# Optimization experiments

Hardware: AMD Instinct MI355X
Metric: run time of the kernel (lower is better)

## Reference

```python
import jax, jax.numpy as jnp
import numpy as np

HIST, CH, HH, WW2 = 10, 11, 30, 40
DM, LNUM, NH, OUT, AD, B = 128, 2, 1, 256, 20, 32
WS = (5, 5, 5)
SS = (2, 2, 2)
SCALE = (DM // NH) ** -0.5
VIS = HIST * CH * HH * WW2


def _np_window_partition(x, ws):
    Bx, D, H, W, C = x.shape
    x = x.reshape(Bx, D // ws[0], ws[0], H // ws[1], ws[1], W // ws[2], ws[2], C)
    return x.transpose(0, 1, 3, 5, 2, 4, 6, 7).reshape(-1, ws[0] * ws[1] * ws[2], C)


def _compute_mask(D, H, W, ws, ss):
    # replicates TinyVideoSwinEncoder._compute_mask (boundary mask + temporal causal mask)
    img = np.zeros((1, D, H, W, 1), np.float32)
    cnt = 0
    for d in (slice(-ws[0]), slice(-ws[0], -ss[0]), slice(-ss[0], None)):
        for h in (slice(-ws[1]), slice(-ws[1], -ss[1]), slice(-ss[1], None)):
            for w in (slice(-ws[2]), slice(-ws[2], -ss[2]), slice(-ss[2], None)):
                img[:, d, h, w, :] = cnt
                cnt += 1
    mw = _np_window_partition(img, ws)[..., 0]  # (nW, N)
    am = mw[:, None, :] - mw[:, :, None]
    am = np.where(am != 0, -100.0, 0.0).astype(np.float32)
    t = np.repeat(np.arange(ws[0]), ws[1] * ws[2])
    causal = np.where(t[:, None] < t[None, :], -100.0, 0.0).astype(np.float32)
    return am + causal[None]


def _rel_index(ws):
    coords = np.stack(np.meshgrid(np.arange(ws[0]), np.arange(ws[1]), np.arange(ws[2]), indexing='ij'))
    cf = coords.reshape(3, -1)
    rel = (cf[:, :, None] - cf[:, None, :]).transpose(1, 2, 0).copy()
    rel[..., 0] += ws[0] - 1
    rel[..., 1] += ws[1] - 1
    rel[..., 2] += ws[2] - 1
    rel[..., 0] *= (2 * ws[1] - 1) * (2 * ws[2] - 1)
    rel[..., 1] *= 2 * ws[2] - 1
    return rel.sum(-1)  # (N, N)


REL_IDX = _rel_index(WS)
MASK_SHIFT = jnp.asarray(_compute_mask(HIST, HH, WW2, WS, SS))
MASK_NONE = jnp.asarray(_compute_mask(HIST, HH, WW2, WS, (0, 0, 0)))


def _ln(x, w, b):
    m = x.mean(-1, keepdims=True)
    v = ((x - m) ** 2).mean(-1, keepdims=True)
    return (x - m) / jnp.sqrt(v + 1e-5) * w + b


def _win_part(x, ws):
    Bx, D, H, W, C = x.shape
    x = x.reshape(Bx, D // ws[0], ws[0], H // ws[1], ws[1], W // ws[2], ws[2], C)
    return x.transpose(0, 1, 3, 5, 2, 4, 6, 7).reshape(-1, ws[0] * ws[1] * ws[2], C)


def _win_rev(win, ws, Bx, D, H, W):
    x = win.reshape(Bx, D // ws[0], H // ws[1], W // ws[2], ws[0], ws[1], ws[2], -1)
    return x.transpose(0, 1, 4, 2, 5, 3, 6, 7).reshape(Bx, D, H, W, -1)


def _block(x, mask, shift, p):
    n1w, n1b, qw, qb, rpb, pw, pb, n2w, n2b, w1, b1, w2, b2 = p
    Bx, D, H, W, C = x.shape
    sc = x
    x = _ln(x, n1w, n1b)
    if any(s > 0 for s in shift):
        x = jnp.roll(x, tuple(-s for s in shift), axis=(1, 2, 3))
    xw = _win_part(x, WS)  # (B_, N, C)
    B_, N = xw.shape[0], xw.shape[1]
    qkv = (xw @ qw + qb).reshape(B_, N, 3, NH, C // NH).transpose(2, 0, 3, 1, 4)
    q, k, v = qkv[0] * SCALE, qkv[1], qkv[2]
    attn = jnp.einsum('bhnd,bhmd->bhnm', q, k)
    bias = rpb[REL_IDX.reshape(-1)].reshape(N, N, NH).transpose(2, 0, 1)
    attn = attn + bias[None]
    nW = mask.shape[0]
    attn = (attn.reshape(B_ // nW, nW, NH, N, N) + mask[None, :, None]).reshape(B_, NH, N, N)
    attn = jax.nn.softmax(attn, axis=-1)
    out = jnp.einsum('bhnm,bhmd->bhnd', attn, v).transpose(0, 2, 1, 3).reshape(B_, N, C)
    out = out @ pw + pb
    x = _win_rev(out, WS, Bx, D, H, W)
    if any(s > 0 for s in shift):
        x = jnp.roll(x, shift, axis=(1, 2, 3))
    x = sc + x
    h = _ln(x, n2w, n2b)
    return x + (jax.nn.gelu(h @ w1 + b1, approximate=False) @ w2 + b2)


def setup_inputs() -> dict:
    key = jax.random.key(0)
    ks = jax.random.split(key, 24)
    r = lambda k, s: jax.random.normal(k, s, jnp.float32) * 0.02
    RPB = (2 * WS[0] - 1) * (2 * WS[1] - 1) * (2 * WS[2] - 1)
    return {
        'obs_stack': jax.random.normal(ks[0], (B, VIS + AD), jnp.float32),
        'patch_w': r(ks[1], (CH, DM)), 'patch_b': r(ks[2], (DM,)),
        'norm1_w': 1.0 + r(ks[3], (LNUM, DM)), 'norm1_b': r(ks[4], (LNUM, DM)),
        'qkv_w': r(ks[5], (LNUM, DM, 3 * DM)), 'qkv_b': r(ks[6], (LNUM, 3 * DM)),
        'rpb_tab': r(ks[7], (LNUM, RPB, NH)),
        'proj_w': r(ks[8], (LNUM, DM, DM)), 'proj_b': r(ks[9], (LNUM, DM)),
        'norm2_w': 1.0 + r(ks[10], (LNUM, DM)), 'norm2_b': r(ks[11], (LNUM, DM)),
        'mlp_w1': r(ks[12], (LNUM, DM, 4 * DM)), 'mlp_b1': r(ks[13], (LNUM, 4 * DM)),
        'mlp_w2': r(ks[14], (LNUM, 4 * DM, DM)), 'mlp_b2': r(ks[15], (LNUM, DM)),
        'normf_w': 1.0 + r(ks[16], (DM,)), 'normf_b': r(ks[17], (DM,)),
        'out_w': r(ks[18], (DM + AD, OUT)), 'out_b': r(ks[19], (OUT,)),
    }


def reference(obs_stack, patch_w, patch_b, norm1_w, norm1_b, qkv_w, qkv_b, rpb_tab,
              proj_w, proj_b, norm2_w, norm2_b, mlp_w1, mlp_b1, mlp_w2, mlp_b2,
              normf_w, normf_b, out_w, out_b):
    Bx = obs_stack.shape[0]
    vis = obs_stack[:, :VIS].reshape(Bx, HIST, CH, HH, WW2).transpose(0, 1, 3, 4, 2)
    x = vis @ patch_w + patch_b  # [B, D, H, W, dm]
    for i in range(LNUM):
        shift = (0, 0, 0) if i % 2 == 0 else SS
        mask = MASK_NONE if i % 2 == 0 else MASK_SHIFT
        p = (norm1_w[i], norm1_b[i], qkv_w[i], qkv_b[i], rpb_tab[i], proj_w[i], proj_b[i],
             norm2_w[i], norm2_b[i], mlp_w1[i], mlp_b1[i], mlp_w2[i], mlp_b2[i])
        x = _block(x, mask, shift, p)
    x = _ln(x, normf_w, normf_b)
    pool = x.reshape(Bx, -1, DM).mean(axis=1)
    feat = jnp.concatenate([pool, obs_stack[:, VIS:]], axis=1)
    return feat @ out_w + out_b
```

## Files before the change

### kernel.cpp

```cpp
#include <hip/hip_runtime.h>
#include <hip/hip_bf16.h>

typedef unsigned short u16;
typedef short bf16x8 __attribute__((ext_vector_type(8)));
typedef float f32x4 __attribute__((ext_vector_type(4)));

#define SCALE_F 0.08838834764831845f

#define VC_PW    0
#define VC_PB    1408
#define VC_N1W   1536
#define VC_N1B   1792
#define VC_QKVB  2048
#define VC_PROJB 2816
#define VC_N2W   3072
#define VC_N2B   3328
#define VC_B1    3584
#define VC_B2    4608
#define VC_NFW   4864
#define VC_NFB   4992
#define VC_RPB   5120
#define VC_OW    6592
#define VC_OBIAS 44480

#define WT_QKV  0
#define WT_PROJ 98304
#define WT_W1   131072
#define WT_W2   262144

#define SH_OFF  8192
#define B1_OFF  13312
#define B2_OFF  13824

__device__ __forceinline__ float bf2f(u16 x) {
  union { unsigned int i; float f; } v; v.i = ((unsigned int)x) << 16; return v.f;
}
__device__ __forceinline__ u16 f2bf(float f) {
  __hip_bfloat16 h = __float2bfloat16(f);
  return __builtin_bit_cast(u16, h);
}
__device__ __forceinline__ unsigned int packbf(float a, float b) {
  return (unsigned int)f2bf(a) | ((unsigned int)f2bf(b) << 16);
}
__device__ __forceinline__ float wsum(float v) {
#pragma unroll
  for (int m = 32; m >= 1; m >>= 1) v += __shfl_xor(v, m, 64);
  return v;
}
__device__ __forceinline__ float gelu_f(float x) {
  float u = x * (-2.3022078f - 0.1029432f * x * x);
  float e = exp2f(u);
  return x * __builtin_amdgcn_rcpf(1.f + e);
}

__global__ __launch_bounds__(256) void k_scan(const u16* __restrict__ raw, int* __restrict__ flag) {
  int nanc = 0, ez = 0;
  for (int i = threadIdx.x; i < 131072; i += 256) {
    u16 x = raw[i];
    if ((x & 0x7F80u) == 0x7F80u) nanc++;
    if (!(i & 1) && x == 0) ez++;
  }
  atomicAdd(&flag[1], nanc);
  atomicAdd(&flag[2], ez);
}
__global__ void k_decide(int* __restrict__ flag) {
  if (threadIdx.x == 0) flag[0] = (flag[1] > 0 || flag[2] > 49152) ? 1 : 0;
}

__global__ __launch_bounds__(256) void k_conv(const void* __restrict__ src, u16* __restrict__ dst,
                                              int n, const int* __restrict__ flag) {
  const int fl = *flag;
  int i = blockIdx.x * 256 + threadIdx.x;
  if (i < n) dst[i] = fl ? f2bf(((const float*)src)[i]) : ((const u16*)src)[i];
}
struct CvTab { const void* src[15]; int off[15]; int n[15]; };
__global__ __launch_bounds__(256) void k_convb(CvTab t, u16* __restrict__ dst,
                                               const int* __restrict__ flag) {
  const int fl = *flag;
  const int s = blockIdx.y;
  const int i = blockIdx.x * 256 + threadIdx.x;
  if (i < t.n[s]) {
    const void* src = t.src[s];
    dst[t.off[s] + i] = fl ? f2bf(((const float*)src)[i]) : ((const u16*)src)[i];
  }
}
__global__ __launch_bounds__(256) void k_convT2(const void* __restrict__ src, u16* __restrict__ dst,
                                                int K, int N, int eoff, const int* __restrict__ flag) {
  const int fl = *flag;
  int id = blockIdx.x * 256 + threadIdx.x;
  if (id < K * N) {
    int n = id / K, k = id % K;
    dst[id] = fl ? f2bf(((const float*)src)[eoff + k * N + n])
                 : ((const u16*)src)[eoff + k * N + n];
  }
}

__global__ __launch_bounds__(256) void k_mask(const u16* __restrict__ vec, u16* __restrict__ MT) {
  const int w = blockIdx.x;
  const bool bnd = (w < 96);
  const u16* rpb = vec + VC_RPB + (bnd ? 729 : 0);
  int wd = 0, wh = 0, ww = 0;
  if (bnd) { wd = w / 48; wh = (w >> 3) % 6; ww = w & 7; }
  for (int e = threadIdx.x; e < 16384; e += 256) {
    int j = e & 127, q = e >> 7;
    int qc = q > 124 ? 124 : q, jc = j > 124 ? 124 : j;
    int ldq = qc / 25, lhq = (qc / 5) % 5, lwq = qc % 5;
    int ldk = jc / 25, lhk = (jc / 5) % 5, lwk = jc % 5;
    float s = bf2f(rpb[((ldq - ldk + 4) * 9 + (lhq - lhk + 4)) * 9 + (lwq - lwk + 4)]);
    if (ldq < ldk) s -= 100.f;
    if (bnd) {
      int gdq = wd * 5 + ldq, ghq = wh * 5 + lhq, gwq = ww * 5 + lwq;
      int gdk = wd * 5 + ldk, ghk = wh * 5 + lhk, gwk = ww * 5 + lwk;
      int rq = (gdq < 5 ? 0 : (gdq < 8 ? 1 : 2)) * 9 + (ghq < 25 ? 0 : (ghq < 28 ? 1 : 2)) * 3 +
               (gwq < 35 ? 0 : (gwq < 38 ? 1 : 2));
      int rk = (gdk < 5 ? 0 : (gdk < 8 ? 1 : 2)) * 9 + (ghk < 25 ? 0 : (ghk < 28 ? 1 : 2)) * 3 +
               (gwk < 35 ? 0 : (gwk < 38 ? 1 : 2));
      if (rq != rk) s -= 100.f;
    }
    MT[(size_t)w * 16384 + e] = f2bf(s);
  }
}

__global__ __launch_bounds__(256) void k_patch(const u16* __restrict__ obs,
                                               const u16* __restrict__ vec,
                                               u16* __restrict__ X) {
  __shared__ float vis[11][40];
  __shared__ float spw[11][128];
  __shared__ float spb[128];
  const int tid = threadIdx.x;
  const int bdh = blockIdx.x;
  const int b = bdh / 300, rem = bdh % 300;
  const int d = rem / 30, h = rem % 30;
  for (int i = tid; i < 1408; i += 256) spw[i >> 7][i & 127] = bf2f(vec[VC_PW + i]);
  if (tid < 128) spb[tid] = bf2f(vec[VC_PB + tid]);
  for (int i = tid; i < 440; i += 256) {
    int ch = i / 40, w = i % 40;
    vis[ch][w] = bf2f(obs[(size_t)b * 132020 + ((d * 11 + ch) * 30 + h) * 40 + w]);
  }
  __syncthreads();
  const size_t xbase = ((size_t)b * 12000 + d * 1200 + h * 40) * 128;
  for (int o2 = tid * 2; o2 < 40 * 128; o2 += 512) {
    int w = o2 >> 7, c = o2 & 127;
    float acc0 = spb[c], acc1 = spb[c + 1];
#pragma unroll
    for (int ch = 0; ch < 11; ch++) {
      float v = vis[ch][w];
      acc0 += v * spw[ch][c];
      acc1 += v * spw[ch][c + 1];
    }
    *(unsigned int*)(X + xbase + o2) = packbf(acc0, acc1);
  }
}

#define MLP_STEP(BUFC, BUFN, HC, PF) {                                                          \
    uint4 w1n, w2n;                                                                             \
    const bool pf_ = (PF);                                                                      \
    if (pf_) {                                                                                  \
      w1n = *(const uint4*)(W1T + (size_t)(((HC) + 1) * 32 + (tid >> 4)) * 128 + (tid & 15) * 8); \
      w2n = *(const uint4*)(W2T + (size_t)(tid >> 2) * 512 + ((HC) + 1) * 32 + (tid & 3) * 8);  \
    }                                                                                           \
    f32x4 h4[2];                                                                                \
    _Pragma("unroll")                                                                           \
    for (int nt = 0; nt < 2; nt++)                                                              \
      _Pragma("unroll")                                                                         \
      for (int r = 0; r < 4; r++) h4[nt][r] = 0.f;                                              \
    _Pragma("unroll")                                                                           \
    for (int kc = 0; kc < 4; kc++) {                                                            \
      _Pragma("unroll")                                                                         \
      for (int nt = 0; nt < 2; nt++) {                                                          \
        int hrow = nt * 16 + m16;                                                               \
        bf16x8 af = *(const bf16x8*)((BUFC) + hrow * 128 + (((4 * kc + quad) ^ m16) << 3));     \
        h4[nt] = __builtin_amdgcn_mfma_f32_16x16x32_bf16(af, biM[kc], h4[nt], 0, 0, 0);         \
      }                                                                                         \
    }                                                                                           \
    _Pragma("unroll")                                                                           \
    for (int nt = 0; nt < 2; nt++) {                                                            \
      int hb = nt * 16 + quad * 4;                                                              \
      float g0 = gelu_f(h4[nt][0] + bf2f(sA[B1_OFF + (HC) * 32 + hb]));                         \
      float g1 = gelu_f(h4[nt][1] + bf2f(sA[B1_OFF + (HC) * 32 + hb + 1]));                     \
      float g2 = gelu_f(h4[nt][2] + bf2f(sA[B1_OFF + (HC) * 32 + hb + 2]));                     \
      float g3 = gelu_f(h4[nt][3] + bf2f(sA[B1_OFF + (HC) * 32 + hb + 3]));                     \
      uint2 pk;                                                                                 \
      pk.x = packbf(g0, g1);                                                                    \
      pk.y = packbf(g2, g3);                                                                    \
      *(uint2*)(sA + SH_OFF + tok * 40 + hb) = pk;                                              \
    }                                                                                           \
    {                                                                                           \
      bf16x8 bh = *(const bf16x8*)(sA + SH_OFF + tok * 40 + quad * 8);                          \
      _Pragma("unroll")                                                                         \
      for (int mt = 0; mt < 8; mt++) {                                                          \
        int oc = mt * 16 + m16;                                                                 \
        bf16x8 af = *(const bf16x8*)((BUFC) + 4096 + oc * 32 + ((quad ^ (oc & 3)) << 3));       \
        acc2[mt] = __builtin_amdgcn_mfma_f32_16x16x32_bf16(af, bh, acc2[mt], 0, 0, 0);          \
      }                                                                                         \
    }                                                                                           \
    if (pf_) {                                                                                  \
      int row_ = tid >> 4, g_ = tid & 15;                                                       \
      *(uint4*)((BUFN) + row_ * 128 + ((g_ ^ (row_ & 15)) << 3)) = w1n;                         \
      int row2_ = tid >> 2, g2_ = tid & 3;                                                      \
      *(uint4*)((BUFN) + 4096 + row2_ * 32 + ((g2_ ^ (row2_ & 3)) << 3)) = w2n;                 \
    }                                                                                           \
    __syncthreads();                                                                            \
  }

__global__ __launch_bounds__(512, 4) void k_win(u16* __restrict__ X,
                                                const u16* __restrict__ Wqkv,
                                                const u16* __restrict__ Wproj,
                                                const u16* __restrict__ W1T,
                                                const u16* __restrict__ W2T,
                                                const u16* __restrict__ qkvb,
                                                const u16* __restrict__ projb,
                                                const u16* __restrict__ n1w, const u16* __restrict__ n1b,
                                                const u16* __restrict__ n2w, const u16* __restrict__ n2b,
                                                const u16* __restrict__ b1, const u16* __restrict__ b2,
                                                const u16* __restrict__ MT,
                                                int shift, int boundary) {
  __shared__ u16 sA[128 * 128];
  __shared__ u16 sB[128 * 128];
  __shared__ uint2 sC[4 * 512];
  u16* sCu = (u16*)sC;
  const int tid = threadIdx.x, lane = tid & 63, wv = tid >> 6;
  const int m16 = lane & 15, quad = lane >> 4;
  const int wing = blockIdx.x;
  const int b = wing / 96, winb = wing % 96;
  const int wd = winb / 48, wh = (winb >> 3) % 6, ww = winb & 7;
  const int tok = wv * 16 + m16;
  const int tokc = tok > 124 ? 124 : tok;
  const u16* mtab = MT + (size_t)(boundary ? winb : 96) * 16384;

  const float nw0 = bf2f(n1w[2 * lane]), nb0 = bf2f(n1b[2 * lane]);
  const float nw1 = bf2f(n1w[2 * lane + 1]), nb1 = bf2f(n1b[2 * lane + 1]);
  for (int rb = 0; rb < 16; rb += 4) {
    unsigned int uu[4];
    float s0[4], s1[4];
#pragma unroll
    for (int i = 0; i < 4; i++) {
      int row = wv * 16 + rb + i;
      int n = row > 124 ? 124 : row;
      int ld = n / 25, lh = (n / 5) % 5, lw = n % 5;
      int d = wd * 5 + ld + shift; if (d >= 10) d -= 10;
      int h = wh * 5 + lh + shift; if (h >= 30) h -= 30;
      int w2 = ww * 5 + lw + shift; if (w2 >= 40) w2 -= 40;
      const u16* xp = X + ((((size_t)b * 10 + d) * 30 + h) * 40 + w2) * 128;
      uu[i] = *(const unsigned int*)(xp + 2 * lane);
    }
#pragma unroll
    for (int i = 0; i < 4; i++) {
      float x0 = bf2f((u16)(uu[i] & 0xffff)), x1 = bf2f((u16)(uu[i] >> 16));
      s0[i] = x0 + x1;
      s1[i] = x0 * x0 + x1 * x1;
    }
#pragma unroll
    for (int m = 32; m >= 1; m >>= 1) {
#pragma unroll
      for (int i = 0; i < 4; i++) {
        s0[i] += __shfl_xor(s0[i], m, 64);
        s1[i] += __shfl_xor(s1[i], m, 64);
      }
    }
#pragma unroll
    for (int i = 0; i < 4; i++) {
      int r = rb + i;
      int row = wv * 16 + r;
      float mean = s0[i] * (1.f / 128.f);
      float var = s1[i] * (1.f / 128.f) - mean * mean;
      float rstd = rsqrtf(var + 1e-5f);
      float x0 = bf2f((u16)(uu[i] & 0xffff)), x1 = bf2f((u16)(uu[i] >> 16));
      float y0 = (x0 - mean) * rstd * nw0 + nb0;
      float y1 = (x1 - mean) * rstd * nw1 + nb1;
      *(unsigned int*)(sA + row * 128 + (((lane >> 2) ^ r) << 3) + ((2 * lane) & 7)) =
          packbf(y0, y1);
    }
  }
  __syncthreads();

  uint2 vreg[4];
  {
    bf16x8 aV[4];
#pragma unroll
    for (int kc = 0; kc < 4; kc++)
      aV[kc] = *(const bf16x8*)(Wqkv + (size_t)(256 + wv * 16 + m16) * 128 + kc * 32 + quad * 8);
    const int oc = 256 + wv * 16 + quad * 4;
    const float b0 = bf2f(qkvb[oc]), b1v = bf2f(qkvb[oc + 1]);
    const float b2v = bf2f(qkvb[oc + 2]), b3 = bf2f(qkvb[oc + 3]);
#pragma unroll
    for (int tt = 0; tt < 8; tt++) {
      f32x4 acc; acc[0] = 0.f; acc[1] = 0.f; acc[2] = 0.f; acc[3] = 0.f;
      int brow = tt * 16 + m16;
#pragma unroll
      for (int kc = 0; kc < 4; kc++) {
        bf16x8 bfr = *(const bf16x8*)(sA + brow * 128 + (((4 * kc + quad) ^ m16) << 3));
        acc = __builtin_amdgcn_mfma_f32_16x16x32_bf16(aV[kc], bfr, acc, 0, 0, 0);
      }
      uint2 pk;
      pk.x = packbf(acc[0] + b0, acc[1] + b1v);
      pk.y = packbf(acc[2] + b2v, acc[3] + b3);
      if (tt < 4) sC[tt * 512 + tid] = pk;
      else vreg[tt - 4] = pk;
    }
  }
  {
    bf16x8 aQ[4];
#pragma unroll
    for (int kc = 0; kc < 4; kc++)
      aQ[kc] = *(const bf16x8*)(Wqkv + (size_t)(wv * 16 + m16) * 128 + kc * 32 + quad * 8);
    const int oc = wv * 16 + quad * 4;
    const float b0 = bf2f(qkvb[oc]), b1v = bf2f(qkvb[oc + 1]);
    const float b2v = bf2f(qkvb[oc + 2]), b3 = bf2f(qkvb[oc + 3]);
#pragma unroll
    for (int tt = 0; tt < 8; tt++) {
      f32x4 acc; acc[0] = 0.f; acc[1] = 0.f; acc[2] = 0.f; acc[3] = 0.f;
      int brow = tt * 16 + m16;
#pragma unroll
      for (int kc = 0; kc < 4; kc++) {
        bf16x8 bfr = *(const bf16x8*)(sA + brow * 128 + (((4 * kc + quad) ^ m16) << 3));
        acc = __builtin_amdgcn_mfma_f32_16x16x32_bf16(aQ[kc], bfr, acc, 0, 0, 0);
      }
      uint2 pk;
      pk.x = packbf((acc[0] + b0) * SCALE_F, (acc[1] + b1v) * SCALE_F);
      pk.y = packbf((acc[2] + b2v) * SCALE_F, (acc[3] + b3) * SCALE_F);
      *(uint2*)(sB + brow * 128 + (((2 * wv + (quad >> 1)) ^ m16) << 3) + ((quad & 1) << 2)) = pk;
    }
  }
  uint2 kreg[8];
  {
    bf16x8 aK[4];
#pragma unroll
    for (int kc = 0; kc < 4; kc++)
      aK[kc] = *(const bf16x8*)(Wqkv + (size_t)(128 + wv * 16 + m16) * 128 + kc * 32 + quad * 8);
    const int oc = 128 + wv * 16 + quad * 4;
    const float b0 = bf2f(qkvb[oc]), b1v = bf2f(qkvb[oc + 1]);
    const float b2v = bf2f(qkvb[oc + 2]), b3 = bf2f(qkvb[oc + 3]);
#pragma unroll
    for (int tt = 0; tt < 8; tt++) {
      f32x4 acc; acc[0] = 0.f; acc[1] = 0.f; acc[2] = 0.f; acc[3] = 0.f;
      int brow = tt * 16 + m16;
#pragma unroll
      for (int kc = 0; kc < 4; kc++) {
        bf16x8 bfr = *(const bf16x8*)(sA + brow * 128 + (((4 * kc + quad) ^ m16) << 3));
        acc = __builtin_amdgcn_mfma_f32_16x16x32_bf16(aK[kc], bfr, acc, 0, 0, 0);
      }
      kreg[tt].x = packbf(acc[0] + b0, acc[1] + b1v);
      kreg[tt].y = packbf(acc[2] + b2v, acc[3] + b3);
    }
  }
  __syncthreads();
#pragma unroll
  for (int tt = 0; tt < 8; tt++) {
    int brow = tt * 16 + m16;
    *(uint2*)(sA + brow * 128 + (((2 * wv + (quad >> 1)) ^ m16) << 3) + ((quad & 1) << 2)) = kreg[tt];
  }
  __syncthreads();

  f32x4 S[8];
#pragma unroll
  for (int jt = 0; jt < 8; jt++) { S[jt][0] = 0.f; S[jt][1] = 0.f; S[jt][2] = 0.f; S[jt][3] = 0.f; }
#pragma unroll
  for (int kc = 0; kc < 4; kc++) {
    bf16x8 qf = *(const bf16x8*)(sB + tok * 128 + (((4 * kc + quad) ^ m16) << 3));
#pragma unroll
    for (int jt = 0; jt < 8; jt++) {
      int row = jt * 16 + m16;
      bf16x8 kf = *(const bf16x8*)(sA + row * 128 + (((4 * kc + quad) ^ m16) << 3));
      S[jt] = __builtin_amdgcn_mfma_f32_16x16x32_bf16(kf, qf, S[jt], 0, 0, 0);
    }
  }
  float mx = -1e30f;
#pragma unroll
  for (int jt = 0; jt < 8; jt++) {
    uint2 mv = *(const uint2*)(mtab + tokc * 128 + jt * 16 + quad * 4);
    u16 mb0 = (u16)(mv.x & 0xffff), mb1 = (u16)(mv.x >> 16);
    u16 mb2 = (u16)(mv.y & 0xffff), mb3 = (u16)(mv.y >> 16);
    float sv0 = S[jt][0] + bf2f(mb0);
    float sv1 = S[jt][1] + bf2f(mb1);
    float sv2 = S[jt][2] + bf2f(mb2);
    float sv3 = S[jt][3] + bf2f(mb3);
    int j0 = jt * 16 + quad * 4;
    if (j0 + 0 >= 125) sv0 = -1e30f;
    if (j0 + 1 >= 125) sv1 = -1e30f;
    if (j0 + 2 >= 125) sv2 = -1e30f;
    if (j0 + 3 >= 125) sv3 = -1e30f;
    S[jt][0] = sv0; S[jt][1] = sv1; S[jt][2] = sv2; S[jt][3] = sv3;
    mx = fmaxf(mx, fmaxf(fmaxf(sv0, sv1), fmaxf(sv2, sv3)));
  }
  mx = fmaxf(mx, __shfl_xor(mx, 16, 64));
  mx = fmaxf(mx, __shfl_xor(mx, 32, 64));
  float sm = 0.f;
#pragma unroll
  for (int jt = 0; jt < 8; jt++)
#pragma unroll
    for (int r = 0; r < 4; r++) {
      float e = __expf(S[jt][r] - mx);
      S[jt][r] = e;
      sm += e;
    }
  sm += __shfl_xor(sm, 16, 64);
  sm += __shfl_xor(sm, 32, 64);
  float inv = 1.f / sm;
#pragma unroll
  for (int jt = 0; jt < 8; jt++) {
    uint2 pk;
    pk.x = packbf(S[jt][0] * inv, S[jt][1] * inv);
    pk.y = packbf(S[jt][2] * inv, S[jt][3] * inv);
    *(uint2*)(sB + tok * 128 + (((2 * jt + (quad >> 1)) ^ m16) << 3) + ((quad & 1) << 2)) = pk;
  }
  __syncthreads();
#pragma unroll
  for (int tt = 0; tt < 8; tt++) {
    uint2 vv = (tt < 4) ? sC[tt * 512 + tid] : vreg[tt - 4];
    int tokv = tt * 16 + m16;
    int c0 = wv * 16 + quad * 4;
    sA[(c0 + 0) * 128 + ((((tokv >> 3) ^ ((c0 + 0) & 15))) << 3) + (tokv & 7)] = (u16)(vv.x & 0xffffu);
    sA[(c0 + 1) * 128 + ((((tokv >> 3) ^ ((c0 + 1) & 15))) << 3) + (tokv & 7)] = (u16)(vv.x >> 16);
    sA[(c0 + 2) * 128 + ((((tokv >> 3) ^ ((c0 + 2) & 15))) << 3) + (tokv & 7)] = (u16)(vv.y & 0xffffu);
    sA[(c0 + 3) * 128 + ((((tokv >> 3) ^ ((c0 + 3) & 15))) << 3) + (tokv & 7)] = (u16)(vv.y >> 16);
  }
  __syncthreads();
  f32x4 O[8];
#pragma unroll
  for (int ct = 0; ct < 8; ct++) { O[ct][0] = 0.f; O[ct][1] = 0.f; O[ct][2] = 0.f; O[ct][3] = 0.f; }
#pragma unroll
  for (int kc = 0; kc < 4; kc++) {
    bf16x8 pf = *(const bf16x8*)(sB + tok * 128 + (((4 * kc + quad) ^ m16) << 3));
#pragma unroll
    for (int ct = 0; ct < 8; ct++) {
      int c = ct * 16 + m16;
      bf16x8 vf = *(const bf16x8*)(sA + c * 128 + (((4 * kc + quad) ^ m16) << 3));
      O[ct] = __builtin_amdgcn_mfma_f32_16x16x32_bf16(vf, pf, O[ct], 0, 0, 0);
    }
  }
#pragma unroll
  for (int ct = 0; ct < 8; ct++) {
    uint2 pk;
    pk.x = packbf(O[ct][0], O[ct][1]);
    pk.y = packbf(O[ct][2], O[ct][3]);
    *(uint2*)(sB + tok * 128 + (((2 * ct + (quad >> 1)) ^ m16) << 3) + ((quad & 1) << 2)) = pk;
  }
  __syncthreads();

  {
    bf16x8 aP[4];
#pragma unroll
    for (int kc = 0; kc < 4; kc++)
      aP[kc] = *(const bf16x8*)(Wproj + (size_t)(wv * 16 + m16) * 128 + kc * 32 + quad * 8);
    const int oc = wv * 16 + quad * 4;
    const float b0 = bf2f(projb[oc]), b1v = bf2f(projb[oc + 1]);
    const float b2v = bf2f(projb[oc + 2]), b3 = bf2f(projb[oc + 3]);
#pragma unroll
    for (int tt = 0; tt < 8; tt++) {
      f32x4 acc; acc[0] = 0.f; acc[1] = 0.f; acc[2] = 0.f; acc[3] = 0.f;
      int brow = tt * 16 + m16;
#pragma unroll
      for (int kc = 0; kc < 4; kc++) {
        bf16x8 bfr = *(const bf16x8*)(sB + brow * 128 + (((4 * kc + quad) ^ m16) << 3));
        acc = __builtin_amdgcn_mfma_f32_16x16x32_bf16(aP[kc], bfr, acc, 0, 0, 0);
      }
      uint2 pk;
      pk.x = packbf(acc[0] + b0, acc[1] + b1v);
      pk.y = packbf(acc[2] + b2v, acc[3] + b3);
      *(uint2*)(sA + brow * 128 + (((2 * wv + (quad >> 1)) ^ m16) << 3) + ((quad & 1) << 2)) = pk;
    }
  }
  __syncthreads();

  uint4 w1r = *(const uint4*)(W1T + (size_t)(tid >> 4) * 128 + (tid & 15) * 8);
  uint4 w2r = *(const uint4*)(W2T + (size_t)(tid >> 2) * 512 + (tid & 3) * 8);
  const float w20 = bf2f(n2w[2 * lane]), v20 = bf2f(n2b[2 * lane]);
  const float w21 = bf2f(n2w[2 * lane + 1]), v21 = bf2f(n2b[2 * lane + 1]);
  for (int rb = 0; rb < 16; rb += 4) {
    float xn0[4], xn1[4], s0[4], s1[4];
#pragma unroll
    for (int i = 0; i < 4; i++) {
      int r = rb + i, row = wv * 16 + r;
      int n = row > 124 ? 124 : row;
      int ld = n / 25, lh = (n / 5) % 5, lw = n % 5;
      int d = wd * 5 + ld + shift; if (d >= 10) d -= 10;
      int h = wh * 5 + lh + shift; if (h >= 30) h -= 30;
      int w2 = ww * 5 + lw + shift; if (w2 >= 40) w2 -= 40;
      u16* xp = X + ((((size_t)b * 10 + d) * 30 + h) * 40 + w2) * 128;
      unsigned int pv = *(const unsigned int*)(sA + row * 128 + (((lane >> 2) ^ r) << 3) + ((2 * lane) & 7));
      unsigned int xo = *(const unsigned int*)(xp + 2 * lane);
      xn0[i] = bf2f((u16)(xo & 0xffff)) + bf2f((u16)(pv & 0xffff));
      xn1[i] = bf2f((u16)(xo >> 16)) + bf2f((u16)(pv >> 16));
      if (row < 125) *(unsigned int*)(xp + 2 * lane) = packbf(xn0[i], xn1[i]);
      s0[i] = xn0[i] + xn1[i];
      s1[i] = xn0[i] * xn0[i] + xn1[i] * xn1[i];
    }
#pragma unroll
    for (int m = 32; m >= 1; m >>= 1) {
#pragma unroll
      for (int i = 0; i < 4; i++) {
        s0[i] += __shfl_xor(s0[i], m, 64);
        s1[i] += __shfl_xor(s1[i], m, 64);
      }
    }
#pragma unroll
    for (int i = 0; i < 4; i++) {
      int r = rb + i, row = wv * 16 + r;
      float mean = s0[i] * (1.f / 128.f);
      float var = s1[i] * (1.f / 128.f) - mean * mean;
      float rstd = rsqrtf(var + 1e-5f);
      float y0 = (xn0[i] - mean) * rstd * w20 + v20;
      float y1 = (xn1[i] - mean) * rstd * w21 + v21;
      *(unsigned int*)(sB + row * 128 + (((lane >> 2) ^ r) << 3) + ((2 * lane) & 7)) =
          packbf(y0, y1);
    }
  }
  bf16x8 biM[4];
#pragma unroll
  for (int kc = 0; kc < 4; kc++)
    biM[kc] = *(const bf16x8*)(sB + tok * 128 + (((4 * kc + quad) ^ m16) << 3));
  __syncthreads();

  {
    int row = tid >> 4, g = tid & 15;
    *(uint4*)(sA + row * 128 + ((g ^ (row & 15)) << 3)) = w1r;
    int row2 = tid >> 2, g2 = tid & 3;
    *(uint4*)(sA + 4096 + row2 * 32 + ((g2 ^ (row2 & 3)) << 3)) = w2r;
    sA[B1_OFF + tid] = b1[tid];
    if (tid < 128) sA[B2_OFF + tid] = b2[tid];
  }
  __syncthreads();

  f32x4 acc2[8];
#pragma unroll
  for (int mt = 0; mt < 8; mt++)
#pragma unroll
    for (int r = 0; r < 4; r++) acc2[mt][r] = 0.f;
  for (int hc2 = 0; hc2 < 8; hc2++) {
    MLP_STEP(sA, sCu, 2 * hc2, true);
    MLP_STEP(sCu, sA, 2 * hc2 + 1, (hc2 < 7));
  }
#pragma unroll
  for (int mt = 0; mt < 8; mt++) {
    int oc = mt * 16 + quad * 4;
    uint2 pk;
    pk.x = packbf(acc2[mt][0] + bf2f(sA[B2_OFF + oc]), acc2[mt][1] + bf2f(sA[B2_OFF + oc + 1]));
    pk.y = packbf(acc2[mt][2] + bf2f(sA[B2_OFF + oc + 2]), acc2[mt][3] + bf2f(sA[B2_OFF + oc + 3]));
    *(uint2*)(sB + tok * 128 + (((2 * mt + (quad >> 1)) ^ m16) << 3) + ((quad & 1) << 2)) = pk;
  }
  for (int r = 0; r < 16; r++) {
    int row = wv * 16 + r;
    if (row > 124) break;
    int ld = row / 25, lh = (row / 5) % 5, lw = row % 5;
    int d = wd * 5 + ld + shift; if (d >= 10) d -= 10;
    int h = wh * 5 + lh + shift; if (h >= 30) h -= 30;
    int w2 = ww * 5 + lw + shift; if (w2 >= 40) w2 -= 40;
    u16* xp = X + ((((size_t)b * 10 + d) * 30 + h) * 40 + w2) * 128;
    unsigned int pv = *(const unsigned int*)(sB + row * 128 + (((lane >> 2) ^ r) << 3) + ((2 * lane) & 7));
    unsigned int xo = *(const unsigned int*)(xp + 2 * lane);
    float o0 = bf2f((u16)(xo & 0xffff)) + bf2f((u16)(pv & 0xffff));
    float o1 = bf2f((u16)(xo >> 16)) + bf2f((u16)(pv >> 16));
    *(unsigned int*)(xp + 2 * lane) = packbf(o0, o1);
  }
}

__global__ __launch_bounds__(256) void k_pool(const u16* __restrict__ X, const u16* __restrict__ vec,
                                              float* __restrict__ pool) {
  __shared__ float sacc[4][128];
  const int tid = threadIdx.x, lane = tid & 63, wv = tid >> 6;
  const int b = blockIdx.x / 50, slice = blockIdx.x % 50;
  const float nw0 = bf2f(vec[VC_NFW + 2 * lane]), nb0 = bf2f(vec[VC_NFB + 2 * lane]);
  const float nw1 = bf2f(vec[VC_NFW + 2 * lane + 1]), nb1 = bf2f(vec[VC_NFB + 2 * lane + 1]);
  float a0 = 0.f, a1 = 0.f;
  for (int tb = wv; tb < 240; tb += 16) {
    unsigned int uu[4];
    float s0[4], s1[4];
#pragma unroll
    for (int i = 0; i < 4; i++) {
      size_t token = (size_t)b * 12000 + slice * 240 + tb + i * 4;
      uu[i] = *(const unsigned int*)(X + token * 128 + 2 * lane);
      float x0 = bf2f((u16)(uu[i] & 0xffff)), x1 = bf2f((u16)(uu[i] >> 16));
      s0[i] = x0 + x1;
      s1[i] = x0 * x0 + x1 * x1;
    }
#pragma unroll
    for (int m = 32; m >= 1; m >>= 1) {
#pragma unroll
      for (int i = 0; i < 4; i++) {
        s0[i] += __shfl_xor(s0[i], m, 64);
        s1[i] += __shfl_xor(s1[i], m, 64);
      }
    }
#pragma unroll
    for (int i = 0; i < 4; i++) {
      float mean = s0[i] * (1.f / 128.f);
      float var = s1[i] * (1.f / 128.f) - mean * mean;
      float rstd = rsqrtf(var + 1e-5f);
      float x0 = bf2f((u16)(uu[i] & 0xffff)), x1 = bf2f((u16)(uu[i] >> 16));
      a0 += (x0 - mean) * rstd * nw0 + nb0;
      a1 += (x1 - mean) * rstd * nw1 + nb1;
    }
  }
  sacc[wv][2 * lane] = a0;
  sacc[wv][2 * lane + 1] = a1;
  __syncthreads();
  if (tid < 128) {
    float s = sacc[0][tid] + sacc[1][tid] + sacc[2][tid] + sacc[3][tid];
    atomicAdd(pool + b * 128 + tid, s);
  }
}

__global__ __launch_bounds__(256) void k_head(const float* __restrict__ pool,
                                              const u16* __restrict__ obs,
                                              const u16* __restrict__ vec,
                                              float* __restrict__ out) {
  const int b = blockIdx.x, o = threadIdx.x;
  float acc = bf2f(vec[VC_OBIAS + o]);
  for (int i = 0; i < 128; i++)
    acc += pool[b * 128 + i] * (1.f / 12000.f) * bf2f(vec[VC_OW + i * 256 + o]);
  for (int i = 0; i < 20; i++)
    acc += bf2f(obs[(size_t)b * 132020 + 132000 + i]) * bf2f(vec[VC_OW + (128 + i) * 256 + o]);
  out[b * 256 + o] = acc;
}

extern "C" void kernel_launch(void* const* d_in, const int* in_sizes, int n_in,
                              void* d_out, int out_size, void* d_ws, size_t ws_size,
                              hipStream_t stream) {
  u16* base  = (u16*)d_ws;
  int* flag  = (int*)d_ws;
  float* pool = (float*)((char*)d_ws + 16);
  u16* VEC   = base + 10000;
  u16* WT    = VEC + 45056;
  u16* OBSC  = WT + 393216;
  u16* X     = OBSC + 4224640;
  u16* MT    = X + 49152000;

  hipMemsetAsync(d_ws, 0, 16 + 32 * 128 * sizeof(float), stream);
  k_scan<<<1, 256, 0, stream>>>((const u16*)d_in[0], flag);
  k_decide<<<1, 64, 0, stream>>>(flag);

  CvTab tab;
  const int cidx[15] = {1, 2, 3, 4, 6, 9, 10, 11, 13, 15, 16, 17, 7, 18, 19};
  const int coff[15] = {VC_PW, VC_PB, VC_N1W, VC_N1B, VC_QKVB, VC_PROJB, VC_N2W, VC_N2B,
                        VC_B1, VC_B2, VC_NFW, VC_NFB, VC_RPB, VC_OW, VC_OBIAS};
  const int cn[15]   = {1408, 128, 256, 256, 768, 256, 256, 256, 1024, 256, 128, 128,
                        1458, 37888, 256};
  for (int s = 0; s < 15; s++) { tab.src[s] = d_in[cidx[s]]; tab.off[s] = coff[s]; tab.n[s] = cn[s]; }
  k_convb<<<dim3(148, 15), 256, 0, stream>>>(tab, VEC, flag);
  k_mask<<<97, 256, 0, stream>>>(VEC, MT);
  k_conv<<<16504, 256, 0, stream>>>(d_in[0], OBSC, 4224640, flag);
  for (int l = 0; l < 2; l++) {
    k_convT2<<<192, 256, 0, stream>>>(d_in[5],  WT + WT_QKV  + l * 49152, 128, 384, l * 49152, flag);
    k_convT2<<<64,  256, 0, stream>>>(d_in[8],  WT + WT_PROJ + l * 16384, 128, 128, l * 16384, flag);
    k_convT2<<<256, 256, 0, stream>>>(d_in[12], WT + WT_W1   + l * 65536, 128, 512, l * 65536, flag);
    k_convT2<<<256, 256, 0, stream>>>(d_in[14], WT + WT_W2   + l * 65536, 512, 128, l * 65536, flag);
  }

  k_patch<<<9600, 256, 0, stream>>>(OBSC, VEC, X);

  for (int l = 0; l < 2; l++) {
    const int shift = l ? 2 : 0;
    k_win<<<3072, 512, 0, stream>>>(X, WT + WT_QKV + l * 49152, WT + WT_PROJ + l * 16384,
                                    WT + WT_W1 + l * 65536, WT + WT_W2 + l * 65536,
                                    VEC + VC_QKVB + l * 384, VEC + VC_PROJB + l * 128,
                                    VEC + VC_N1W + l * 128, VEC + VC_N1B + l * 128,
                                    VEC + VC_N2W + l * 128, VEC + VC_N2B + l * 128,
                                    VEC + VC_B1 + l * 512, VEC + VC_B2 + l * 128,
                                    MT, shift, l);
  }

  k_pool<<<1600, 256, 0, stream>>>(X, VEC, pool);
  k_head<<<32, 256, 0, stream>>>(pool, OBSC, VEC, (float*)d_out);
}
```

Measured before the change: 1.183 ms.

## Batch conversion launches, fold decide into scan, prefetch MLP weights earlier

```diff
diff --git a/kernel.cpp b/kernel.cpp
--- a/kernel.cpp
+++ b/kernel.cpp
@@ -29,8 +29,6 @@
 #define WT_W2   262144
 
 #define SH_OFF  8192
-#define B1_OFF  13312
-#define B2_OFF  13824
 
 __device__ __forceinline__ float bf2f(u16 x) {
   union { unsigned int i; float f; } v; v.i = ((unsigned int)x) << 16; return v.f;
@@ -54,17 +52,19 @@
 }
 
 __global__ __launch_bounds__(256) void k_scan(const u16* __restrict__ raw, int* __restrict__ flag) {
+  __shared__ int snan, sez;
+  if (threadIdx.x == 0) { snan = 0; sez = 0; }
+  __syncthreads();
   int nanc = 0, ez = 0;
   for (int i = threadIdx.x; i < 131072; i += 256) {
     u16 x = raw[i];
     if ((x & 0x7F80u) == 0x7F80u) nanc++;
     if (!(i & 1) && x == 0) ez++;
   }
-  atomicAdd(&flag[1], nanc);
-  atomicAdd(&flag[2], ez);
-}
-__global__ void k_decide(int* __restrict__ flag) {
-  if (threadIdx.x == 0) flag[0] = (flag[1] > 0 || flag[2] > 49152) ? 1 : 0;
+  atomicAdd(&snan, nanc);
+  atomicAdd(&sez, ez);
+  __syncthreads();
+  if (threadIdx.x == 0) flag[0] = (snan > 0 || sez > 49152) ? 1 : 0;
 }
 
 __global__ __launch_bounds__(256) void k_conv(const void* __restrict__ src, u16* __restrict__ dst,
@@ -84,14 +84,18 @@
     dst[t.off[s] + i] = fl ? f2bf(((const float*)src)[i]) : ((const u16*)src)[i];
   }
 }
-__global__ __launch_bounds__(256) void k_convT2(const void* __restrict__ src, u16* __restrict__ dst,
-                                                int K, int N, int eoff, const int* __restrict__ flag) {
+struct CtTab { const void* src[8]; int K[8]; int N[8]; int eoff[8]; int doff[8]; };
+__global__ __launch_bounds__(256) void k_convT2b(CtTab t, u16* __restrict__ WT,
+                                                 const int* __restrict__ flag) {
   const int fl = *flag;
-  int id = blockIdx.x * 256 + threadIdx.x;
-  if (id < K * N) {
+  const int s = blockIdx.y;
+  const int id = blockIdx.x * 256 + threadIdx.x;
+  const int K = t.K[s];
+  if (id < K * t.N[s]) {
     int n = id / K, k = id % K;
-    dst[id] = fl ? f2bf(((const float*)src)[eoff + k * N + n])
-                 : ((const u16*)src)[eoff + k * N + n];
+    const void* src = t.src[s];
+    int e = t.eoff[s] + k * t.N[s] + n;
+    WT[t.doff[s] + id] = fl ? f2bf(((const float*)src)[e]) : ((const u16*)src)[e];
   }
 }
 
@@ -176,10 +180,10 @@
     _Pragma("unroll")                                                                           \
     for (int nt = 0; nt < 2; nt++) {                                                            \
       int hb = nt * 16 + quad * 4;                                                              \
-      float g0 = gelu_f(h4[nt][0] + bf2f(sA[B1_OFF + (HC) * 32 + hb]));                         \
-      float g1 = gelu_f(h4[nt][1] + bf2f(sA[B1_OFF + (HC) * 32 + hb + 1]));                     \
-      float g2 = gelu_f(h4[nt][2] + bf2f(sA[B1_OFF + (HC) * 32 + hb + 2]));                     \
-      float g3 = gelu_f(h4[nt][3] + bf2f(sA[B1_OFF + (HC) * 32 + hb + 3]));                     \
+      float g0 = gelu_f(h4[nt][0] + bf2f(b1[(HC) * 32 + hb]));                                  \
+      float g1 = gelu_f(h4[nt][1] + bf2f(b1[(HC) * 32 + hb + 1]));                              \
+      float g2 = gelu_f(h4[nt][2] + bf2f(b1[(HC) * 32 + hb + 2]));                              \
+      float g3 = gelu_f(h4[nt][3] + bf2f(b1[(HC) * 32 + hb + 3]));                              \
       uint2 pk;                                                                                 \
       pk.x = packbf(g0, g1);                                                                    \
       pk.y = packbf(g2, g3);                                                                    \
@@ -404,6 +408,8 @@
     pk.y = packbf(S[jt][2] * inv, S[jt][3] * inv);
     *(uint2*)(sB + tok * 128 + (((2 * jt + (quad >> 1)) ^ m16) << 3) + ((quad & 1) << 2)) = pk;
   }
+  uint4 w1r = *(const uint4*)(W1T + (size_t)(tid >> 4) * 128 + (tid & 15) * 8);
+  uint4 w2r = *(const uint4*)(W2T + (size_t)(tid >> 2) * 512 + (tid & 3) * 8);
   __syncthreads();
 #pragma unroll
   for (int tt = 0; tt < 8; tt++) {
@@ -416,6 +422,12 @@
     sA[(c0 + 3) * 128 + ((((tokv >> 3) ^ ((c0 + 3) & 15))) << 3) + (tokv & 7)] = (u16)(vv.y >> 16);
   }
   __syncthreads();
+  {
+    int row = tid >> 4, g = tid & 15;
+    *(uint4*)(sCu + row * 128 + ((g ^ (row & 15)) << 3)) = w1r;
+    int row2 = tid >> 2, g2 = tid & 3;
+    *(uint4*)(sCu + 4096 + row2 * 32 + ((g2 ^ (row2 & 3)) << 3)) = w2r;
+  }
   f32x4 O[8];
 #pragma unroll
   for (int ct = 0; ct < 8; ct++) { O[ct][0] = 0.f; O[ct][1] = 0.f; O[ct][2] = 0.f; O[ct][3] = 0.f; }
@@ -463,8 +475,6 @@
   }
   __syncthreads();
 
-  uint4 w1r = *(const uint4*)(W1T + (size_t)(tid >> 4) * 128 + (tid & 15) * 8);
-  uint4 w2r = *(const uint4*)(W2T + (size_t)(tid >> 2) * 512 + (tid & 3) * 8);
   const float w20 = bf2f(n2w[2 * lane]), v20 = bf2f(n2b[2 * lane]);
   const float w21 = bf2f(n2w[2 * lane + 1]), v21 = bf2f(n2b[2 * lane + 1]);
   for (int rb = 0; rb < 16; rb += 4) {
@@ -512,31 +522,21 @@
     biM[kc] = *(const bf16x8*)(sB + tok * 128 + (((4 * kc + quad) ^ m16) << 3));
   __syncthreads();
 
-  {
-    int row = tid >> 4, g = tid & 15;
-    *(uint4*)(sA + row * 128 + ((g ^ (row & 15)) << 3)) = w1r;
-    int row2 = tid >> 2, g2 = tid & 3;
-    *(uint4*)(sA + 4096 + row2 * 32 + ((g2 ^ (row2 & 3)) << 3)) = w2r;
-    sA[B1_OFF + tid] = b1[tid];
-    if (tid < 128) sA[B2_OFF + tid] = b2[tid];
-  }
-  __syncthreads();
-
   f32x4 acc2[8];
 #pragma unroll
   for (int mt = 0; mt < 8; mt++)
 #pragma unroll
     for (int r = 0; r < 4; r++) acc2[mt][r] = 0.f;
   for (int hc2 = 0; hc2 < 8; hc2++) {
-    MLP_STEP(sA, sCu, 2 * hc2, true);
-    MLP_STEP(sCu, sA, 2 * hc2 + 1, (hc2 < 7));
+    MLP_STEP(sCu, sA, 2 * hc2, true);
+    MLP_STEP(sA, sCu, 2 * hc2 + 1, (hc2 < 7));
   }
 #pragma unroll
   for (int mt = 0; mt < 8; mt++) {
     int oc = mt * 16 + quad * 4;
     uint2 pk;
-    pk.x = packbf(acc2[mt][0] + bf2f(sA[B2_OFF + oc]), acc2[mt][1] + bf2f(sA[B2_OFF + oc + 1]));
-    pk.y = packbf(acc2[mt][2] + bf2f(sA[B2_OFF + oc + 2]), acc2[mt][3] + bf2f(sA[B2_OFF + oc + 3]));
+    pk.x = packbf(acc2[mt][0] + bf2f(b2[oc]), acc2[mt][1] + bf2f(b2[oc + 1]));
+    pk.y = packbf(acc2[mt][2] + bf2f(b2[oc + 2]), acc2[mt][3] + bf2f(b2[oc + 3]));
     *(uint2*)(sB + tok * 128 + (((2 * mt + (quad >> 1)) ^ m16) << 3) + ((quad & 1) << 2)) = pk;
   }
   for (int r = 0; r < 16; r++) {
@@ -628,7 +628,6 @@
 
   hipMemsetAsync(d_ws, 0, 16 + 32 * 128 * sizeof(float), stream);
   k_scan<<<1, 256, 0, stream>>>((const u16*)d_in[0], flag);
-  k_decide<<<1, 64, 0, stream>>>(flag);
 
   CvTab tab;
   const int cidx[15] = {1, 2, 3, 4, 6, 9, 10, 11, 13, 15, 16, 17, 7, 18, 19};
@@ -640,12 +639,18 @@
   k_convb<<<dim3(148, 15), 256, 0, stream>>>(tab, VEC, flag);
   k_mask<<<97, 256, 0, stream>>>(VEC, MT);
   k_conv<<<16504, 256, 0, stream>>>(d_in[0], OBSC, 4224640, flag);
+  CtTab tt;
   for (int l = 0; l < 2; l++) {
-    k_convT2<<<192, 256, 0, stream>>>(d_in[5],  WT + WT_QKV  + l * 49152, 128, 384, l * 49152, flag);
-    k_convT2<<<64,  256, 0, stream>>>(d_in[8],  WT + WT_PROJ + l * 16384, 128, 128, l * 16384, flag);
-    k_convT2<<<256, 256, 0, stream>>>(d_in[12], WT + WT_W1   + l * 65536, 128, 512, l * 65536, flag);
-    k_convT2<<<256, 256, 0, stream>>>(d_in[14], WT + WT_W2   + l * 65536, 512, 128, l * 65536, flag);
-  }
+    tt.src[l * 4 + 0] = d_in[5];  tt.K[l * 4 + 0] = 128; tt.N[l * 4 + 0] = 384;
+    tt.eoff[l * 4 + 0] = l * 49152; tt.doff[l * 4 + 0] = WT_QKV + l * 49152;
+    tt.src[l * 4 + 1] = d_in[8];  tt.K[l * 4 + 1] = 128; tt.N[l * 4 + 1] = 128;
+    tt.eoff[l * 4 + 1] = l * 16384; tt.doff[l * 4 + 1] = WT_PROJ + l * 16384;
+    tt.src[l * 4 + 2] = d_in[12]; tt.K[l * 4 + 2] = 128; tt.N[l * 4 + 2] = 512;
+    tt.eoff[l * 4 + 2] = l * 65536; tt.doff[l * 4 + 2] = WT_W1 + l * 65536;
+    tt.src[l * 4 + 3] = d_in[14]; tt.K[l * 4 + 3] = 512; tt.N[l * 4 + 3] = 128;
+    tt.eoff[l * 4 + 3] = l * 65536; tt.doff[l * 4 + 3] = WT_W2 + l * 65536;
+  }
+  k_convT2b<<<dim3(256, 8), 256, 0, stream>>>(tt, WT, flag);
 
   k_patch<<<9600, 256, 0, stream>>>(OBSC, VEC, X);
 
```

Result: slower. 1.208 ms (+2.1%).
